# Performance work log

Hardware: AMD Instinct MI355X
Metric: run time of the kernel (lower is better)

Reference implementation:

```python
import jax, jax.numpy as jnp
import numpy as np

LOG2 = float(np.log(2.0))

def ssp(x):
    # shifted softplus: ln(0.5*exp(x) + 0.5) = softplus(x) - ln(2)
    return jax.nn.softplus(x) - LOG2

N, A, F, R, E = 50000, 128, 128, 20, 1600000

def setup_inputs() -> dict:
    key = jax.random.key(0)
    ks = jax.random.split(key, 14)
    s = lambda fan_in: 1.0 / np.sqrt(fan_in)
    return {
        "x": jax.random.normal(ks[0], (N, A), dtype=jnp.float32),
        "f_ij": jax.random.uniform(ks[1], (E, R), dtype=jnp.float32),
        "rcut_ij": jax.random.uniform(ks[2], (E,), dtype=jnp.float32),
        "idx_i": jnp.sort(jax.random.randint(ks[3], (E,), 0, N)),
        "idx_j": jax.random.randint(ks[4], (E,), 0, N),
        # in2f: Dense(A -> F), no bias
        "W_in2f": jax.random.uniform(ks[5], (A, F), minval=-s(A), maxval=s(A), dtype=jnp.float32),
        # filter_network: Dense(R->F, ssp) then Dense(F->F)
        "W_f1": jax.random.uniform(ks[6], (R, F), minval=-s(R), maxval=s(R), dtype=jnp.float32),
        "b_f1": jnp.zeros((F,), dtype=jnp.float32),
        "W_f2": jax.random.uniform(ks[7], (F, F), minval=-s(F), maxval=s(F), dtype=jnp.float32),
        "b_f2": jnp.zeros((F,), dtype=jnp.float32),
        # f2out: Dense(F->A, ssp) then Dense(A->A)
        "W_o1": jax.random.uniform(ks[8], (F, A), minval=-s(F), maxval=s(F), dtype=jnp.float32),
        "b_o1": jnp.zeros((A,), dtype=jnp.float32),
        "W_o2": jax.random.uniform(ks[9], (A, A), minval=-s(A), maxval=s(A), dtype=jnp.float32),
        "b_o2": jnp.zeros((A,), dtype=jnp.float32),
    }

def reference(x, f_ij, rcut_ij, idx_i, idx_j,
              W_in2f, W_f1, b_f1, W_f2, b_f2, W_o1, b_o1, W_o2, b_o2):
    n_atoms = x.shape[0]
    # in2f projection (no bias): [N, A] -> [N, F]
    h = x @ W_in2f
    # filter MLP on edge RBF features: [E, R] -> [E, F]
    Wij = ssp(f_ij @ W_f1 + b_f1) @ W_f2 + b_f2
    Wij = Wij * rcut_ij[:, None]
    # gather neighbor features, modulate by filter, scatter-add to centers
    x_ij = h[idx_j] * Wij                                   # [E, F]
    agg = jax.ops.segment_sum(x_ij, idx_i, num_segments=n_atoms)  # [N, F]
    # f2out MLP: [N, F] -> [N, A]
    out = ssp(agg @ W_o1 + b_o1) @ W_o2 + b_o2
    return out
```

## Files before the change

### kernel.cpp

```cpp
#include <hip/hip_runtime.h>
#include <math.h>

#define LN2F 0.6931471805599453f
#define LOG2EF 1.4426950408889634f

typedef _Float16 half_t;
typedef _Float16 half4_t __attribute__((ext_vector_type(4)));
typedef _Float16 half8_t __attribute__((ext_vector_type(8)));
typedef __fp16 fp16x2 __attribute__((ext_vector_type(2)));
typedef __fp16 fp16x4 __attribute__((ext_vector_type(4)));
typedef float f32x4 __attribute__((ext_vector_type(4)));

__device__ __forceinline__ float sspf(float z) {
    return fmaxf(z, 0.f) + __logf(1.f + __expf(-fabsf(z))) - LN2F;
}
__device__ __forceinline__ half4_t cvt4(float x, float y, float z, float w) {
    half4_t r; r[0]=(half_t)x; r[1]=(half_t)y; r[2]=(half_t)z; r[3]=(half_t)w; return r;
}
__device__ __forceinline__ half4_t pk4(float a, float b, float c, float d) {
    fp16x2 lo = __builtin_amdgcn_cvt_pkrtz(a, b);
    fp16x2 hi = __builtin_amdgcn_cvt_pkrtz(c, d);
    fp16x4 v = __builtin_shufflevector(lo, hi, 0, 1, 2, 3);
    return __builtin_bit_cast(half4_t, v);
}

__device__ __forceinline__ void load_lds16(const void* g, void* l) {
    __builtin_amdgcn_global_load_lds(
        (const __attribute__((address_space(1))) unsigned int*)g,
        (__attribute__((address_space(3))) unsigned int*)l, 16, 0, 0);
}

__device__ __forceinline__ int lbound(const int* __restrict__ a, int n, int key) {
    int lo = 0, hi = n;
    while (lo < hi) { int m = (lo + hi) >> 1; if (a[m] < key) lo = m + 1; else hi = m; }
    return lo;
}

__global__ __launch_bounds__(256) void prep_weights(
    const float* __restrict__ W_in2f, const float* __restrict__ W_f2,
    const float* __restrict__ W_o1, const float* __restrict__ W_o2,
    const float* __restrict__ b_f1, const float* __restrict__ b_f2,
    half_t* __restrict__ Wt_in2f, half_t* __restrict__ W2L,
    half_t* __restrict__ Wt_o1, half_t* __restrict__ Wt_o2,
    float* __restrict__ b1sc, float* __restrict__ b2a)
{
    int b = blockIdx.x;
    if (b < 64) {
        int i = b*256 + threadIdx.x;
        Wt_in2f[i] = (half_t)W_in2f[(i & 127)*128 + (i >> 7)];
    } else if (b < 128) {
        int i = (b-64)*256 + threadIdx.x;
        int j = i & 3, s = (i >> 2) & 1, ln = (i >> 3) & 15;
        int g = (i >> 7) & 3, m = (i >> 9) & 3, kk = i >> 11;
        W2L[i] = (half_t)(LN2F * W_f2[(kk*16 + g*4 + j)*128 + (2*m+s)*16 + ln]);
    } else if (b < 192) {
        int i = (b-128)*256 + threadIdx.x;
        Wt_o1[i] = (half_t)W_o1[(i & 127)*128 + (i >> 7)];
    } else if (b < 256) {
        int i = (b-192)*256 + threadIdx.x;
        Wt_o2[i] = (half_t)W_o2[(i & 127)*128 + (i >> 7)];
    } else {
        int c = threadIdx.x;
        if (c < 128) {
            float s = 0.f;
            for (int k = 0; k < 128; ++k) s += W_f2[k*128 + c];
            b2a[c]  = b_f2[c] - LN2F * s;
            b1sc[c] = b_f1[c] * LOG2EF;
        }
    }
}

__global__ __launch_bounds__(256) void seg_starts(
    const int* __restrict__ idx_i, int* __restrict__ atom_start, int E, int N)
{
    int e = blockIdx.x * 256 + threadIdx.x;
    if (e >= E) return;
    int a = idx_i[e];
    int prev = (e == 0) ? -1 : idx_i[e - 1];
    for (int k = prev + 1; k <= a; ++k) atom_start[k] = e;
    if (e == E - 1)
        for (int k = a + 1; k <= N; ++k) atom_start[k] = E;
}

__global__ __launch_bounds__(256) void mfma_gemm_h(
    const float* __restrict__ A, const half_t* __restrict__ Bt,
    half_t* __restrict__ Ch, int nrows)
{
    const int tid = threadIdx.x;
    const int w = tid >> 6, l = tid & 63, g = l >> 4, ln = l & 15;
    const int r0 = blockIdx.x * 64;

    f32x4 acc[4][2];
    #pragma unroll
    for (int rf = 0; rf < 4; ++rf)
        #pragma unroll
        for (int cf = 0; cf < 2; ++cf) acc[rf][cf] = (f32x4)0.f;

    #pragma unroll
    for (int kk = 0; kk < 8; ++kk) {
        const int kb = kk * 16 + g * 4;
        half4_t a[4];
        #pragma unroll
        for (int rf = 0; rf < 4; ++rf) {
            int r = r0 + rf * 16 + ln;
            int rr = r < nrows ? r : nrows - 1;
            float4 av = *(const float4*)(A + (size_t)rr * 128 + kb);
            a[rf] = cvt4(av.x, av.y, av.z, av.w);
        }
        #pragma unroll
        for (int cf = 0; cf < 2; ++cf) {
            int n = w * 32 + cf * 16 + ln;
            half4_t b = *(const half4_t*)(Bt + (size_t)n * 128 + kb);
            #pragma unroll
            for (int rf = 0; rf < 4; ++rf)
                acc[rf][cf] = __builtin_amdgcn_mfma_f32_16x16x16f16(a[rf], b, acc[rf][cf], 0, 0, 0);
        }
    }
    #pragma unroll
    for (int cf = 0; cf < 2; ++cf) {
        int n = w * 32 + cf * 16 + ln;
        #pragma unroll
        for (int rf = 0; rf < 4; ++rf)
            #pragma unroll
            for (int reg = 0; reg < 4; ++reg) {
                int r = r0 + rf * 16 + g * 4 + reg;
                if (r < nrows) Ch[(size_t)r * 128 + n] = (half_t)acc[rf][cf][reg];
            }
    }
}

__global__ __launch_bounds__(256) void mfma_gemm2(
    const float* __restrict__ A, const half_t* __restrict__ Bt1,
    const float* __restrict__ bias1, const half_t* __restrict__ Bt2,
    const float* __restrict__ bias2, float* __restrict__ out, int nrows)
{
    __shared__ half_t ts[64][136];
    const int tid = threadIdx.x;
    const int w = tid >> 6, l = tid & 63, g = l >> 4, ln = l & 15;
    const int r0 = blockIdx.x * 64;

    f32x4 acc[4][2];
    #pragma unroll
    for (int rf = 0; rf < 4; ++rf)
        #pragma unroll
        for (int cf = 0; cf < 2; ++cf) acc[rf][cf] = (f32x4)0.f;
    #pragma unroll
    for (int kk = 0; kk < 8; ++kk) {
        const int kb = kk * 16 + g * 4;
        half4_t a[4];
        #pragma unroll
        for (int rf = 0; rf < 4; ++rf) {
            int r = r0 + rf * 16 + ln;
            int rr = r < nrows ? r : nrows - 1;
            float4 av = *(const float4*)(A + (size_t)rr * 128 + kb);
            a[rf] = cvt4(av.x, av.y, av.z, av.w);
        }
        #pragma unroll
        for (int cf = 0; cf < 2; ++cf) {
            int n = w * 32 + cf * 16 + ln;
            half4_t b = *(const half4_t*)(Bt1 + (size_t)n * 128 + kb);
            #pragma unroll
            for (int rf = 0; rf < 4; ++rf)
                acc[rf][cf] = __builtin_amdgcn_mfma_f32_16x16x16f16(a[rf], b, acc[rf][cf], 0, 0, 0);
        }
    }
    #pragma unroll
    for (int cf = 0; cf < 2; ++cf) {
        int n = w * 32 + cf * 16 + ln;
        float bv = bias1[n];
        #pragma unroll
        for (int rf = 0; rf < 4; ++rf)
            #pragma unroll
            for (int reg = 0; reg < 4; ++reg)
                ts[rf*16 + g*4 + reg][n] = (half_t)sspf(acc[rf][cf][reg] + bv);
    }
    __syncthreads();

    f32x4 acc2[4][2];
    #pragma unroll
    for (int rf = 0; rf < 4; ++rf)
        #pragma unroll
        for (int cf = 0; cf < 2; ++cf) acc2[rf][cf] = (f32x4)0.f;
    #pragma unroll
    for (int kk = 0; kk < 8; ++kk) {
        const int kb = kk * 16 + g * 4;
        half4_t a[4];
        #pragma unroll
        for (int rf = 0; rf < 4; ++rf)
            a[rf] = *(const half4_t*)&ts[rf*16 + ln][kb];
        #pragma unroll
        for (int cf = 0; cf < 2; ++cf) {
            int n = w * 32 + cf * 16 + ln;
            half4_t b = *(const half4_t*)(Bt2 + (size_t)n * 128 + kb);
            #pragma unroll
            for (int rf = 0; rf < 4; ++rf)
                acc2[rf][cf] = __builtin_amdgcn_mfma_f32_16x16x16f16(a[rf], b, acc2[rf][cf], 0, 0, 0);
        }
    }
    #pragma unroll
    for (int cf = 0; cf < 2; ++cf) {
        int n = w * 32 + cf * 16 + ln;
        float bv = bias2[n];
        #pragma unroll
        for (int rf = 0; rf < 4; ++rf)
            #pragma unroll
            for (int reg = 0; reg < 4; ++reg) {
                int r = r0 + rf * 16 + g * 4 + reg;
                if (r < nrows) out[(size_t)r * 128 + n] = acc2[rf][cf][reg] + bv;
            }
    }
}

__global__ __launch_bounds__(256, 2) void edge_kernel(
    const float* __restrict__ f_ij, const float* __restrict__ rcut,
    const int* __restrict__ idx_j,
    const float* __restrict__ W_f1, const float* __restrict__ b1sc,
    const half_t* __restrict__ W2L, const float* __restrict__ b2a,
    const half_t* __restrict__ hh, float* __restrict__ agg,
    const int* __restrict__ atom_start, int E, int N, int W)
{
    __shared__ __align__(16) half_t W2s[16384];
    __shared__ __align__(16) half_t hsh[4][2][2048];
    __shared__ __align__(16) half_t W1s[128][24];
    __shared__ float b1s[128];

    const int tid = threadIdx.x;
    const int w = tid >> 6, l = tid & 63, g = l >> 4, ln = l & 15;
    const int lnh = ln >> 3, lnlo = ln & 7;

    for (int i = tid; i < 2048; i += 256)
        ((float4*)W2s)[i] = ((const float4*)W2L)[i];
    for (int i = tid; i < 128*24; i += 256) {
        int f = i / 24, k = i - f*24;
        W1s[f][k] = (k < 20) ? (half_t)W_f1[k*128 + f] : (half_t)0.f;
    }
    if (tid < 128) b1s[tid] = b1sc[tid];
    __syncthreads();

    const int kg = blockIdx.x * 4 + w;
    const int aLo = lbound(atom_start, N + 1, (int)((size_t)kg * E / W));
    const int aHi = (kg == W - 1) ? N
                  : lbound(atom_start, N + 1, (int)((size_t)(kg + 1) * E / W));
    if (aLo >= aHi) return;

    float b2v[8];
    #pragma unroll
    for (int q = 0; q < 8; ++q) b2v[q] = b2a[q*16 + ln];

    int acur = aLo;
    int ends0 = atom_start[acur + 1];
    int ends1 = atom_start[min(acur + 2, N)];
    int ends2 = atom_start[min(acur + 3, N)];
    int cs = atom_start[acur];
    int ce = min(cs + 16, ends0);
    bool fl0 = (ce == ends0);
    int csn = ce;
    int cen = min(csn + 16, fl0 ? ends1 : ends0);

    int jvN[4];
    {
        int jv0[4];
        #pragma unroll
        for (int it = 0; it < 4; ++it)
            jv0[it] = idx_j[min(cs + 4*it + g, E - 1)];
        asm volatile("" ::: "memory");
        #pragma unroll
        for (int it = 0; it < 4; ++it)
            load_lds16(hh + (size_t)jv0[it]*128 + ((ln ^ (2*it)) << 3),
                       &hsh[w][0][it*512]);
        asm volatile("" ::: "memory");
    }
    float4 fA, fB;
    {
        int e = min(cs + ln, E - 1);
        fA = *(const float4*)(f_ij + (size_t)e*20 + g*4);
        fB = *(const float4*)(f_ij + (size_t)e*20 + 16);
    }
    float rc[4];
    #pragma unroll
    for (int r2 = 0; r2 < 4; ++r2) rc[r2] = rcut[min(cs + 4*g + r2, E - 1)];
    #pragma unroll
    for (int it = 0; it < 4; ++it) jvN[it] = idx_j[min(csn + 4*it + g, E - 1)];
    asm volatile("" ::: "memory");

    float racc[8];
    #pragma unroll
    for (int q = 0; q < 8; ++q) racc[q] = 0.f;
    int p = 0;

    while (acur < aHi) {
        asm volatile("" ::: "memory");
        #pragma unroll
        for (int it = 0; it < 4; ++it)
            load_lds16(hh + (size_t)jvN[it]*128 + ((ln ^ (2*it)) << 3),
                       &hsh[w][p^1][it*512]);
        asm volatile("s_waitcnt vmcnt(4)" ::: "memory");
        __builtin_amdgcn_sched_barrier(0);

        half4_t bfr0 = cvt4(fA.x, fA.y, fA.z, fA.w);
        half4_t bfr1;
        if (g == 0) bfr1 = cvt4(fB.x, fB.y, fB.z, fB.w);
        else { half4_t zz = {}; bfr1 = zz; }
        float rcm[4];
        #pragma unroll
        for (int r2 = 0; r2 < 4; ++r2)
            rcm[r2] = (cs + 4*g + r2 < ce) ? rc[r2] : 0.f;
        const bool flushF = (ce == ends0);
        const bool f1 = (cen == (flushF ? ends1 : ends0));
        const int cs2 = cen;
        const int endsel = flushF ? (f1 ? ends2 : ends1) : (f1 ? ends1 : ends0);
        const int ce2 = min(cs2 + 16, endsel);

        int jv2[4];
        #pragma unroll
        for (int it = 0; it < 4; ++it)
            jv2[it] = idx_j[min(cs2 + 4*it + g, E - 1)];
        float4 fA1, fB1;
        {
            int e = min(csn + ln, E - 1);
            fA1 = *(const float4*)(f_ij + (size_t)e*20 + g*4);
            fB1 = *(const float4*)(f_ij + (size_t)e*20 + 16);
        }
        float rc1[4];
        #pragma unroll
        for (int r2 = 0; r2 < 4; ++r2) rc1[r2] = rcut[min(csn + 4*g + r2, E - 1)];
        const int aeL = atom_start[min(acur + 4, N)];
        asm volatile("" ::: "memory");

        half4_t a2[8];
        #pragma unroll
        for (int rf = 0; rf < 8; ++rf) {
            f32x4 z = (f32x4)0.f;
            half4_t a0f = *(const half4_t*)&W1s[rf*16 + ln][g*4];
            z = __builtin_amdgcn_mfma_f32_16x16x16f16(a0f, bfr0, z, 0, 0, 0);
            half4_t a1f;
            if (g == 0) a1f = *(const half4_t*)&W1s[rf*16 + ln][16];
            else { half4_t zz = {}; a1f = zz; }
            z = __builtin_amdgcn_mfma_f32_16x16x16f16(a1f, bfr1, z, 0, 0, 0);
            float4 bb = *(const float4*)&b1s[rf*16 + g*4];
            float l0 = __log2f(1.f + exp2f(fmaf(z[0], LOG2EF, bb.x)));
            float l1 = __log2f(1.f + exp2f(fmaf(z[1], LOG2EF, bb.y)));
            float l2 = __log2f(1.f + exp2f(fmaf(z[2], LOG2EF, bb.z)));
            float l3 = __log2f(1.f + exp2f(fmaf(z[3], LOG2EF, bb.w)));
            a2[rf] = pk4(l0, l1, l2, l3);
        }

        f32x4 acc[4];
        #pragma unroll
        for (int q = 0; q < 4; ++q) { f32x4 t = {b2v[q], b2v[q], b2v[q], b2v[q]}; acc[q] = t; }
        __builtin_amdgcn_s_setprio(1);
        #pragma unroll
        for (int kk = 0; kk < 8; ++kk)
            #pragma unroll
            for (int m = 0; m < 2; ++m) {
                half8_t bw = *(const half8_t*)&W2s[(((kk*4 + m)*4 + g)*16 + ln)*8];
                half4_t blo = __builtin_shufflevector(bw, bw, 0, 1, 2, 3);
                half4_t bhi = __builtin_shufflevector(bw, bw, 4, 5, 6, 7);
                acc[2*m]   = __builtin_amdgcn_mfma_f32_16x16x16f16(a2[kk], blo, acc[2*m],   0, 0, 0);
                acc[2*m+1] = __builtin_amdgcn_mfma_f32_16x16x16f16(a2[kk], bhi, acc[2*m+1], 0, 0, 0);
            }
        __builtin_amdgcn_s_setprio(0);

        #pragma unroll
        for (int q = 0; q < 4; ++q) {
            float s = 0.f;
            #pragma unroll
            for (int r2 = 0; r2 < 4; ++r2) {
                int segp = (2*q + lnh) ^ (2*g);
                float hv = (float)hsh[w][p][(4*g + r2)*128 + segp*8 + lnlo];
                s = fmaf(acc[q][r2] * rcm[r2], hv, s);
            }
            racc[q] += s;
        }

        #pragma unroll
        for (int q = 0; q < 4; ++q) { f32x4 t = {b2v[4+q], b2v[4+q], b2v[4+q], b2v[4+q]}; acc[q] = t; }
        __builtin_amdgcn_s_setprio(1);
        #pragma unroll
        for (int kk = 0; kk < 8; ++kk)
            #pragma unroll
            for (int m = 2; m < 4; ++m) {
                half8_t bw = *(const half8_t*)&W2s[(((kk*4 + m)*4 + g)*16 + ln)*8];
                half4_t blo = __builtin_shufflevector(bw, bw, 0, 1, 2, 3);
                half4_t bhi = __builtin_shufflevector(bw, bw, 4, 5, 6, 7);
                acc[2*(m-2)]   = __builtin_amdgcn_mfma_f32_16x16x16f16(a2[kk], blo, acc[2*(m-2)],   0, 0, 0);
                acc[2*(m-2)+1] = __builtin_amdgcn_mfma_f32_16x16x16f16(a2[kk], bhi, acc[2*(m-2)+1], 0, 0, 0);
            }
        __builtin_amdgcn_s_setprio(0);
        #pragma unroll
        for (int q = 0; q < 4; ++q) {
            int nt = 4 + q;
            float s = 0.f;
            #pragma unroll
            for (int r2 = 0; r2 < 4; ++r2) {
                int segp = (2*nt + lnh) ^ (2*g);
                float hv = (float)hsh[w][p][(4*g + r2)*128 + segp*8 + lnlo];
                s = fmaf(acc[q][r2] * rcm[r2], hv, s);
            }
            racc[nt] += s;
        }

        if (flushF) {
            #pragma unroll
            for (int q = 0; q < 8; ++q) {
                float r = racc[q];
                r += __shfl_xor(r, 16, 64);
                r += __shfl_xor(r, 32, 64);
                racc[q] = r;
            }
            if (g == 0) {
                #pragma unroll
                for (int q = 0; q < 8; ++q)
                    agg[(size_t)acur*128 + q*16 + ln] = racc[q];
            }
            #pragma unroll
            for (int q = 0; q < 8; ++q) racc[q] = 0.f;
            ++acur;
            ends0 = ends1; ends1 = ends2; ends2 = aeL;
        }

        cs = csn; ce = cen; csn = cs2; cen = ce2;
        #pragma unroll
        for (int it = 0; it < 4; ++it) jvN[it] = jv2[it];
        fA = fA1; fB = fB1;
        #pragma unroll
        for (int r2 = 0; r2 < 4; ++r2) rc[r2] = rc1[r2];
        p ^= 1;
    }
}

extern "C" void kernel_launch(void* const* d_in, const int* in_sizes, int n_in,
                              void* d_out, int out_size, void* d_ws, size_t ws_size,
                              hipStream_t stream)
{
    const float* x      = (const float*)d_in[0];
    const float* f_ij   = (const float*)d_in[1];
    const float* rcut   = (const float*)d_in[2];
    const int*   idx_i  = (const int*)d_in[3];
    const int*   idx_j  = (const int*)d_in[4];
    const float* W_in2f = (const float*)d_in[5];
    const float* W_f1   = (const float*)d_in[6];
    const float* b_f1   = (const float*)d_in[7];
    const float* W_f2   = (const float*)d_in[8];
    const float* b_f2   = (const float*)d_in[9];
    const float* W_o1   = (const float*)d_in[10];
    const float* b_o1   = (const float*)d_in[11];
    const float* W_o2   = (const float*)d_in[12];
    const float* b_o2   = (const float*)d_in[13];

    const int N = in_sizes[0] / 128;
    const int E = in_sizes[2];

    half_t* h16  = (half_t*)d_ws;
    half_t* wt   = (half_t*)((char*)d_ws + (size_t)N * 128 * 4);
    half_t* Wt_in2f = wt;
    half_t* W2L     = wt + 16384;
    half_t* Wt_o1   = W2L + 16384;
    half_t* Wt_o2   = Wt_o1 + 16384;
    float*  b1sc    = (float*)(Wt_o2 + 16384);
    float*  b2a     = b1sc + 128;
    int* atom_start = (int*)(b2a + 128);

    prep_weights<<<257, 256, 0, stream>>>(W_in2f, W_f2, W_o1, W_o2, b_f1, b_f2,
                                          Wt_in2f, W2L, Wt_o1, Wt_o2, b1sc, b2a);
    seg_starts<<<(E + 255) / 256, 256, 0, stream>>>(idx_i, atom_start, E, N);

    const int gn  = (N + 63) / 64;
    const int nbl = 512;
    const int W   = nbl * 4;

    mfma_gemm_h<<<gn, 256, 0, stream>>>(x, Wt_in2f, h16, N);

    edge_kernel<<<nbl, 256, 0, stream>>>(f_ij, rcut, idx_j,
                                         W_f1, b1sc, W2L, b2a,
                                         h16, (float*)d_out, atom_start, E, N, W);

    mfma_gemm2<<<gn, 256, 0, stream>>>((const float*)d_out, Wt_o1, b_o1,
                                       Wt_o2, b_o2, (float*)d_out, N);
}
```

Measured before the change: 306.5 us.

## Switch edge filter MLP to 16x16x32 f16 MFMA with register-resident W_f1

Replaces the 16x16x16 f16 MFMAs in the edge kernel's two filter layers with the gfx950 16x16x32 f16 instruction, which halves the MFMA instruction count per K. W2L is re-laid out in prep_weights to match the new operand packing, and activations are packed eight halves at a time. W_f1 is now transposed and padded to K=32 in prep_weights and held in registers per wave, replacing the per-block LDS staging and the LDS reads inside the loop. In exchange, register pressure rises and a 273rd block plus an extra buffer are added to the prep step.

```diff
diff --git a/kernel.cpp b/kernel.cpp
--- a/kernel.cpp
+++ b/kernel.cpp
@@ -9,6 +9,7 @@
 typedef _Float16 half8_t __attribute__((ext_vector_type(8)));
 typedef __fp16 fp16x2 __attribute__((ext_vector_type(2)));
 typedef __fp16 fp16x4 __attribute__((ext_vector_type(4)));
+typedef __fp16 fp16x8 __attribute__((ext_vector_type(8)));
 typedef float f32x4 __attribute__((ext_vector_type(4)));
 
 __device__ __forceinline__ float sspf(float z) {
@@ -17,11 +18,16 @@
 __device__ __forceinline__ half4_t cvt4(float x, float y, float z, float w) {
     half4_t r; r[0]=(half_t)x; r[1]=(half_t)y; r[2]=(half_t)z; r[3]=(half_t)w; return r;
 }
-__device__ __forceinline__ half4_t pk4(float a, float b, float c, float d) {
-    fp16x2 lo = __builtin_amdgcn_cvt_pkrtz(a, b);
-    fp16x2 hi = __builtin_amdgcn_cvt_pkrtz(c, d);
-    fp16x4 v = __builtin_shufflevector(lo, hi, 0, 1, 2, 3);
-    return __builtin_bit_cast(half4_t, v);
+__device__ __forceinline__ half8_t pk8(float a, float b, float c, float d,
+                                       float e, float f, float g, float h) {
+    fp16x2 p0 = __builtin_amdgcn_cvt_pkrtz(a, b);
+    fp16x2 p1 = __builtin_amdgcn_cvt_pkrtz(c, d);
+    fp16x2 p2 = __builtin_amdgcn_cvt_pkrtz(e, f);
+    fp16x2 p3 = __builtin_amdgcn_cvt_pkrtz(g, h);
+    fp16x4 lo = __builtin_shufflevector(p0, p1, 0, 1, 2, 3);
+    fp16x4 hi = __builtin_shufflevector(p2, p3, 0, 1, 2, 3);
+    fp16x8 v  = __builtin_shufflevector(lo, hi, 0, 1, 2, 3, 4, 5, 6, 7);
+    return __builtin_bit_cast(half8_t, v);
 }
 
 __device__ __forceinline__ void load_lds16(const void* g, void* l) {
@@ -37,27 +43,33 @@
 }
 
 __global__ __launch_bounds__(256) void prep_weights(
-    const float* __restrict__ W_in2f, const float* __restrict__ W_f2,
-    const float* __restrict__ W_o1, const float* __restrict__ W_o2,
+    const float* __restrict__ W_in2f, const float* __restrict__ W_f1,
+    const float* __restrict__ W_f2, const float* __restrict__ W_o1,
+    const float* __restrict__ W_o2,
     const float* __restrict__ b_f1, const float* __restrict__ b_f2,
-    half_t* __restrict__ Wt_in2f, half_t* __restrict__ W2L,
-    half_t* __restrict__ Wt_o1, half_t* __restrict__ Wt_o2,
-    float* __restrict__ b1sc, float* __restrict__ b2a)
+    half_t* __restrict__ Wt_in2f, half_t* __restrict__ Wt_f1,
+    half_t* __restrict__ W2L, half_t* __restrict__ Wt_o1,
+    half_t* __restrict__ Wt_o2, float* __restrict__ b1sc, float* __restrict__ b2a)
 {
     int b = blockIdx.x;
     if (b < 64) {
         int i = b*256 + threadIdx.x;
         Wt_in2f[i] = (half_t)W_in2f[(i & 127)*128 + (i >> 7)];
-    } else if (b < 128) {
+    } else if (b < 80) {
         int i = (b-64)*256 + threadIdx.x;
-        int j = i & 3, s = (i >> 2) & 1, ln = (i >> 3) & 15;
-        int g = (i >> 7) & 3, m = (i >> 9) & 3, kk = i >> 11;
-        W2L[i] = (half_t)(LN2F * W_f2[(kk*16 + g*4 + j)*128 + (2*m+s)*16 + ln]);
-    } else if (b < 192) {
-        int i = (b-128)*256 + threadIdx.x;
+        int n = i >> 5, k = i & 31;
+        Wt_f1[i] = (k < 20) ? (half_t)W_f1[k*128 + n] : (half_t)0.f;
+    } else if (b < 144) {
+        int i = (b-80)*256 + threadIdx.x;
+        int j = i & 7, ln = (i >> 3) & 15, g = (i >> 7) & 3;
+        int nt = (i >> 9) & 7, t = i >> 12;
+        int k = 32*t + ((j < 4) ? (g*4 + j) : (16 + g*4 + (j - 4)));
+        W2L[i] = (half_t)(LN2F * W_f2[k*128 + nt*16 + ln]);
+    } else if (b < 208) {
+        int i = (b-144)*256 + threadIdx.x;
         Wt_o1[i] = (half_t)W_o1[(i & 127)*128 + (i >> 7)];
-    } else if (b < 256) {
-        int i = (b-192)*256 + threadIdx.x;
+    } else if (b < 272) {
+        int i = (b-208)*256 + threadIdx.x;
         Wt_o2[i] = (half_t)W_o2[(i & 127)*128 + (i >> 7)];
     } else {
         int c = threadIdx.x;
@@ -214,14 +226,13 @@
 __global__ __launch_bounds__(256, 2) void edge_kernel(
     const float* __restrict__ f_ij, const float* __restrict__ rcut,
     const int* __restrict__ idx_j,
-    const float* __restrict__ W_f1, const float* __restrict__ b1sc,
+    const half_t* __restrict__ Wt_f1, const float* __restrict__ b1sc,
     const half_t* __restrict__ W2L, const float* __restrict__ b2a,
     const half_t* __restrict__ hh, float* __restrict__ agg,
     const int* __restrict__ atom_start, int E, int N, int W)
 {
     __shared__ __align__(16) half_t W2s[16384];
     __shared__ __align__(16) half_t hsh[4][2][2048];
-    __shared__ __align__(16) half_t W1s[128][24];
     __shared__ float b1s[128];
 
     const int tid = threadIdx.x;
@@ -230,10 +241,6 @@
 
     for (int i = tid; i < 2048; i += 256)
         ((float4*)W2s)[i] = ((const float4*)W2L)[i];
-    for (int i = tid; i < 128*24; i += 256) {
-        int f = i / 24, k = i - f*24;
-        W1s[f][k] = (k < 20) ? (half_t)W_f1[k*128 + f] : (half_t)0.f;
-    }
     if (tid < 128) b1s[tid] = b1sc[tid];
     __syncthreads();
 
@@ -242,6 +249,14 @@
     const int aHi = (kg == W - 1) ? N
                   : lbound(atom_start, N + 1, (int)((size_t)(kg + 1) * E / W));
     if (aLo >= aHi) return;
+
+    half8_t w1f[8];
+    #pragma unroll
+    for (int rf = 0; rf < 8; ++rf) {
+        half4_t lo = *(const half4_t*)(Wt_f1 + (size_t)(rf*16 + ln)*32 + g*4);
+        half4_t hi = *(const half4_t*)(Wt_f1 + (size_t)(rf*16 + ln)*32 + 16 + g*4);
+        w1f[rf] = __builtin_shufflevector(lo, hi, 0, 1, 2, 3, 4, 5, 6, 7);
+    }
 
     float b2v[8];
     #pragma unroll
@@ -297,10 +312,11 @@
         asm volatile("s_waitcnt vmcnt(4)" ::: "memory");
         __builtin_amdgcn_sched_barrier(0);
 
-        half4_t bfr0 = cvt4(fA.x, fA.y, fA.z, fA.w);
-        half4_t bfr1;
-        if (g == 0) bfr1 = cvt4(fB.x, fB.y, fB.z, fB.w);
-        else { half4_t zz = {}; bfr1 = zz; }
+        half4_t blo = cvt4(fA.x, fA.y, fA.z, fA.w);
+        half4_t bhi;
+        if (g == 0) bhi = cvt4(fB.x, fB.y, fB.z, fB.w);
+        else { half4_t zz = {}; bhi = zz; }
+        half8_t bf = __builtin_shufflevector(blo, bhi, 0, 1, 2, 3, 4, 5, 6, 7);
         float rcm[4];
         #pragma unroll
         for (int r2 = 0; r2 < 4; ++r2)
@@ -327,22 +343,24 @@
         const int aeL = atom_start[min(acur + 4, N)];
         asm volatile("" ::: "memory");
 
-        half4_t a2[8];
-        #pragma unroll
-        for (int rf = 0; rf < 8; ++rf) {
-            f32x4 z = (f32x4)0.f;
-            half4_t a0f = *(const half4_t*)&W1s[rf*16 + ln][g*4];
-            z = __builtin_amdgcn_mfma_f32_16x16x16f16(a0f, bfr0, z, 0, 0, 0);
-            half4_t a1f;
-            if (g == 0) a1f = *(const half4_t*)&W1s[rf*16 + ln][16];
-            else { half4_t zz = {}; a1f = zz; }
-            z = __builtin_amdgcn_mfma_f32_16x16x16f16(a1f, bfr1, z, 0, 0, 0);
-            float4 bb = *(const float4*)&b1s[rf*16 + g*4];
-            float l0 = __log2f(1.f + exp2f(fmaf(z[0], LOG2EF, bb.x)));
-            float l1 = __log2f(1.f + exp2f(fmaf(z[1], LOG2EF, bb.y)));
-            float l2 = __log2f(1.f + exp2f(fmaf(z[2], LOG2EF, bb.z)));
-            float l3 = __log2f(1.f + exp2f(fmaf(z[3], LOG2EF, bb.w)));
-            a2[rf] = pk4(l0, l1, l2, l3);
+        f32x4 z[8];
+        #pragma unroll
+        for (int rf = 0; rf < 8; ++rf)
+            z[rf] = __builtin_amdgcn_mfma_f32_16x16x32_f16(w1f[rf], bf, (f32x4)0.f, 0, 0, 0);
+        half8_t a2[4];
+        #pragma unroll
+        for (int t = 0; t < 4; ++t) {
+            float4 bbA = *(const float4*)&b1s[(2*t)*16 + g*4];
+            float4 bbB = *(const float4*)&b1s[(2*t+1)*16 + g*4];
+            float l0 = __log2f(1.f + exp2f(fmaf(z[2*t][0],   LOG2EF, bbA.x)));
+            float l1 = __log2f(1.f + exp2f(fmaf(z[2*t][1],   LOG2EF, bbA.y)));
+            float l2 = __log2f(1.f + exp2f(fmaf(z[2*t][2],   LOG2EF, bbA.z)));
+            float l3 = __log2f(1.f + exp2f(fmaf(z[2*t][3],   LOG2EF, bbA.w)));
+            float l4 = __log2f(1.f + exp2f(fmaf(z[2*t+1][0], LOG2EF, bbB.x)));
+            float l5 = __log2f(1.f + exp2f(fmaf(z[2*t+1][1], LOG2EF, bbB.y)));
+            float l6 = __log2f(1.f + exp2f(fmaf(z[2*t+1][2], LOG2EF, bbB.z)));
+            float l7 = __log2f(1.f + exp2f(fmaf(z[2*t+1][3], LOG2EF, bbB.w)));
+            a2[t] = pk8(l0, l1, l2, l3, l4, l5, l6, l7);
         }
 
         f32x4 acc[4];
@@ -350,14 +368,11 @@
         for (int q = 0; q < 4; ++q) { f32x4 t = {b2v[q], b2v[q], b2v[q], b2v[q]}; acc[q] = t; }
         __builtin_amdgcn_s_setprio(1);
         #pragma unroll
-        for (int kk = 0; kk < 8; ++kk)
-            #pragma unroll
-            for (int m = 0; m < 2; ++m) {
-                half8_t bw = *(const half8_t*)&W2s[(((kk*4 + m)*4 + g)*16 + ln)*8];
-                half4_t blo = __builtin_shufflevector(bw, bw, 0, 1, 2, 3);
-                half4_t bhi = __builtin_shufflevector(bw, bw, 4, 5, 6, 7);
-                acc[2*m]   = __builtin_amdgcn_mfma_f32_16x16x16f16(a2[kk], blo, acc[2*m],   0, 0, 0);
-                acc[2*m+1] = __builtin_amdgcn_mfma_f32_16x16x16f16(a2[kk], bhi, acc[2*m+1], 0, 0, 0);
+        for (int t = 0; t < 4; ++t)
+            #pragma unroll
+            for (int q = 0; q < 4; ++q) {
+                half8_t bw = *(const half8_t*)&W2s[(((t*8 + q)*4 + g)*16 + ln)*8];
+                acc[q] = __builtin_amdgcn_mfma_f32_16x16x32_f16(a2[t], bw, acc[q], 0, 0, 0);
             }
         __builtin_amdgcn_s_setprio(0);
 
@@ -377,14 +392,11 @@
         for (int q = 0; q < 4; ++q) { f32x4 t = {b2v[4+q], b2v[4+q], b2v[4+q], b2v[4+q]}; acc[q] = t; }
         __builtin_amdgcn_s_setprio(1);
         #pragma unroll
-        for (int kk = 0; kk < 8; ++kk)
-            #pragma unroll
-            for (int m = 2; m < 4; ++m) {
-                half8_t bw = *(const half8_t*)&W2s[(((kk*4 + m)*4 + g)*16 + ln)*8];
-                half4_t blo = __builtin_shufflevector(bw, bw, 0, 1, 2, 3);
-                half4_t bhi = __builtin_shufflevector(bw, bw, 4, 5, 6, 7);
-                acc[2*(m-2)]   = __builtin_amdgcn_mfma_f32_16x16x16f16(a2[kk], blo, acc[2*(m-2)],   0, 0, 0);
-                acc[2*(m-2)+1] = __builtin_amdgcn_mfma_f32_16x16x16f16(a2[kk], bhi, acc[2*(m-2)+1], 0, 0, 0);
+        for (int t = 0; t < 4; ++t)
+            #pragma unroll
+            for (int q = 0; q < 4; ++q) {
+                half8_t bw = *(const half8_t*)&W2s[(((t*8 + 4 + q)*4 + g)*16 + ln)*8];
+                acc[q] = __builtin_amdgcn_mfma_f32_16x16x32_f16(a2[t], bw, acc[q], 0, 0, 0);
             }
         __builtin_amdgcn_s_setprio(0);
         #pragma unroll
@@ -454,15 +466,18 @@
     half_t* h16  = (half_t*)d_ws;
     half_t* wt   = (half_t*)((char*)d_ws + (size_t)N * 128 * 4);
     half_t* Wt_in2f = wt;
-    half_t* W2L     = wt + 16384;
+    half_t* Wt_f1   = wt + 16384;
+    half_t* W2L     = wt + 16384 + 4096;
     half_t* Wt_o1   = W2L + 16384;
     half_t* Wt_o2   = Wt_o1 + 16384;
     float*  b1sc    = (float*)(Wt_o2 + 16384);
     float*  b2a     = b1sc + 128;
     int* atom_start = (int*)(b2a + 128);
 
-    prep_weights<<<257, 256, 0, stream>>>(W_in2f, W_f2, W_o1, W_o2, b_f1, b_f2,
-                                          Wt_in2f, W2L, Wt_o1, Wt_o2, b1sc, b2a);
+    prep_weights<<<273, 256, 0, stream>>>(W_in2f, W_f1, W_f2, W_o1, W_o2,
+                                          b_f1, b_f2,
+                                          Wt_in2f, Wt_f1, W2L, Wt_o1, Wt_o2,
+                                          b1sc, b2a);
     seg_starts<<<(E + 255) / 256, 256, 0, stream>>>(idx_i, atom_start, E, N);
 
     const int gn  = (N + 63) / 64;
@@ -472,7 +487,7 @@
     mfma_gemm_h<<<gn, 256, 0, stream>>>(x, Wt_in2f, h16, N);
 
     edge_kernel<<<nbl, 256, 0, stream>>>(f_ij, rcut, idx_j,
-                                         W_f1, b1sc, W2L, b2a,
+                                         Wt_f1, b1sc, W2L, b2a,
                                          h16, (float*)d_out, atom_start, E, N, W);
 
     mfma_gemm2<<<gn, 256, 0, stream>>>((const float*)d_out, Wt_o1, b_o1,
```

Result: faster. 267.4 us (-12.8%).
